# Optimization experiments

Measured on AMD Instinct MI355X. Metric: run time of the kernel, lower is better.

## Reference

```python
import jax, jax.numpy as jnp
import numpy as np

B, D_IN, D_HID, D_OUT = 32768, 512, 1024, 2048

def setup_inputs() -> dict:
    key = jax.random.key(0)
    k1, k2, k3, k4 = jax.random.split(key, 4)
    x = jax.random.normal(k1, (B, D_IN), dtype=jnp.float32)
    # linear1 params (torch Linear default-style init, scale approximated)
    l1_w = jax.random.normal(k2, (D_HID, D_IN), dtype=jnp.float32) * (D_IN ** -0.5)
    l1_b = jax.random.normal(k3, (D_HID,), dtype=jnp.float32) * 0.01
    # second linear params: normal(0, hidden^-0.5) weight, zero bias as in source
    weight = jax.random.normal(k4, (D_OUT, D_HID), dtype=jnp.float32) * (D_HID ** -0.5)
    bias = jnp.zeros((D_OUT,), dtype=jnp.float32)
    return {"x": x, "l1_w": l1_w, "l1_b": l1_b, "weight": weight, "bias": bias}

def reference(x, l1_w, l1_b, weight, bias):
    # linear1: [B, D_IN] -> [B, D_HID]
    h = jnp.einsum('bi,hi->bh', x, l1_w) + l1_b
    # fused linear + max epilogue: scores [B, D_OUT] -> max over output dim
    scores = jnp.einsum('bh,oh->bo', h, weight) + bias
    return jnp.max(scores, axis=-1)  # [B]
```

## Files before the change

### kernel.cpp

```cpp
#include <hip/hip_runtime.h>
#include <hip/hip_bf16.h>
#include <stdint.h>

static constexpr int BATCH = 32768;
static constexpr int DIN   = 512;
static constexpr int DHID  = 1024;
static constexpr int DOUT  = 2048;

typedef __bf16 bf16x8 __attribute__((ext_vector_type(8)));
typedef float  f32x4  __attribute__((ext_vector_type(4)));

__device__ __forceinline__ unsigned short f2bf(float f) {
    unsigned int u = __float_as_uint(f);
    u += 0x7FFFu + ((u >> 16) & 1u);
    return (unsigned short)(u >> 16);
}

__device__ __forceinline__ void gload_lds16(const void* g, void* l) {
    __builtin_amdgcn_global_load_lds((__attribute__((address_space(1))) void*)g,
                                     (__attribute__((address_space(3))) void*)l,
                                     16, 0, 0);
}


__global__ __launch_bounds__(256) void prep_kernel(
    const float* __restrict__ w1, const float4* __restrict__ w2,
    unsigned short* __restrict__ w1t, ushort4* __restrict__ w2b) {
    if (blockIdx.x < 512) {
        __shared__ float tile[32][33];
        const int t     = threadIdx.x;
        const int tileI = blockIdx.x & 15;
        const int tileH = blockIdx.x >> 4;
        const int iBase = tileI * 32, hBase = tileH * 32;
        const int col = t & 31, rowq = t >> 5;
#pragma unroll
        for (int p = 0; p < 4; ++p) {
            const int row = p * 8 + rowq;
            tile[row][col] = w1[(size_t)(hBase + row) * DIN + iBase + col];
        }
        __syncthreads();
#pragma unroll
        for (int p = 0; p < 4; ++p) {
            const int row = p * 8 + rowq;
            w1t[(size_t)(iBase + row) * DHID + hBase + col] = f2bf(tile[col][row]);
        }
    } else {
        const size_t g = (size_t)(blockIdx.x - 512) * 256 + threadIdx.x;
        float4 v = w2[g];
        ushort4 o;
        o.x = f2bf(v.x); o.y = f2bf(v.y); o.z = f2bf(v.z); o.w = f2bf(v.w);
        w2b[g] = o;
    }
}

__global__ __launch_bounds__(256) void bgemv_kernel(
    const float* __restrict__ w2, const float* __restrict__ b1,
    const float* __restrict__ b2, float* __restrict__ bp) {
    const int o    = blockIdx.x * 4 + (threadIdx.x >> 6);
    const int lane = threadIdx.x & 63;
    const float* row = w2 + (size_t)o * DHID;
    float s = 0.f;
#pragma unroll
    for (int j = 0; j < 16; ++j) {
        const int h = j * 64 + lane;
        s += row[h] * b1[h];
    }
#pragma unroll
    for (int off = 1; off < 64; off <<= 1) s += __shfl_xor(s, off);
    if (lane == 0) bp[o] = s + b2[o];
}

__global__ __launch_bounds__(256) void gemmW_kernel(
    const unsigned short* __restrict__ A,
    const unsigned short* __restrict__ Bw,
    unsigned short* __restrict__ W) {
    constexpr int K = DHID;
    __shared__ __align__(16) unsigned short sA[128 * 64];
    __shared__ __align__(16) unsigned short sB[128 * 64];

    const int tid  = threadIdx.x;
    const int lane = tid & 63;
    const int wid  = tid >> 6;
    const int wr = wid >> 1, wc = wid & 1;
    const int r = lane & 15, q = lane >> 4;
    const int sw = r & 7;
    const int blockN = blockIdx.x * 128;
    const int blockM = blockIdx.y * 128;

    const int chKey = (lane & 7) ^ ((lane >> 3) & 7);
    const size_t aBase = (size_t)(blockM + wid * 32 + (lane >> 3)) * K + chKey * 8;
    const size_t bBase = (size_t)(blockN + wid * 32 + (lane >> 3)) * K + chKey * 8;

    f32x4 acc[4][4];
#pragma unroll
    for (int mt = 0; mt < 4; ++mt)
#pragma unroll
        for (int nt = 0; nt < 4; ++nt) { f32x4 z = {0.f, 0.f, 0.f, 0.f}; acc[mt][nt] = z; }

    for (int k0 = 0; k0 < K; k0 += 64) {
#pragma unroll
        for (int j = 0; j < 4; ++j) {
            gload_lds16(A  + aBase + (size_t)j * 8 * K + k0, sA + wid * 2048 + j * 512);
            gload_lds16(Bw + bBase + (size_t)j * 8 * K + k0, sB + wid * 2048 + j * 512);
        }
        __syncthreads();
#pragma unroll
        for (int ks = 0; ks < 2; ++ks) {
            const int ch = ((ks << 2) + q) ^ sw;
            bf16x8 af[4], bf[4];
#pragma unroll
            for (int mt = 0; mt < 4; ++mt) af[mt] = *(const bf16x8*)&sA[(wr * 64 + mt * 16 + r) * 64 + ch * 8];
#pragma unroll
            for (int nt = 0; nt < 4; ++nt) bf[nt] = *(const bf16x8*)&sB[(wc * 64 + nt * 16 + r) * 64 + ch * 8];
#pragma unroll
            for (int mt = 0; mt < 4; ++mt)
#pragma unroll
                for (int nt = 0; nt < 4; ++nt)
                    acc[mt][nt] = __builtin_amdgcn_mfma_f32_16x16x32_bf16(af[mt], bf[nt], acc[mt][nt], 0, 0, 0);
        }
        __syncthreads();
    }

    const int colBase = blockN + wc * 64;
    const int rowBase = blockM + wr * 64;
#pragma unroll
    for (int mt = 0; mt < 4; ++mt) {
        const int row0 = rowBase + mt * 16 + q * 4;
#pragma unroll
        for (int nt = 0; nt < 4; ++nt) {
            const int col = colBase + nt * 16 + r;
#pragma unroll
            for (int reg = 0; reg < 4; ++reg)
                W[(size_t)(row0 + reg) * DIN + col] = f2bf(acc[mt][nt][reg]);
        }
    }
}

__global__ __launch_bounds__(256) void gemmS_kernel(
    const float* __restrict__ X,
    const unsigned short* __restrict__ Bw,
    const float* __restrict__ bp,
    float* __restrict__ partials,
    int mBase) {
    constexpr int K = DIN;
    __shared__ __align__(16) unsigned short sA[128 * 64];
    __shared__ __align__(16) unsigned short sB[128 * 64];

    const int tid  = threadIdx.x;
    const int lane = tid & 63;
    const int wid  = tid >> 6;
    const int wr = wid >> 1, wc = wid & 1;
    const int r = lane & 15, q = lane >> 4;
    const int sw = r & 7;

    const int g    = blockIdx.x;
    const int xcd  = g & 7;
    const int i    = g >> 3;
    const int nIdx = i & 15;
    const int blockM = mBase + (xcd * 16 + (i >> 4)) * 128;
    const int blockN = nIdx * 128;

    int aRow[4], aCh[4], aSlot[4];
#pragma unroll
    for (int j = 0; j < 4; ++j) {
        const int u = j * 256 + tid;
        aRow[j]  = u >> 3;
        aCh[j]   = u & 7;
        aSlot[j] = aRow[j] * 8 + (aCh[j] ^ (aRow[j] & 7));
    }
    const int chKey = (lane & 7) ^ ((lane >> 3) & 7);
    const size_t bBase = (size_t)(blockN + wid * 32 + (lane >> 3)) * K + chKey * 8;

    f32x4 acc[4][4];
#pragma unroll
    for (int mt = 0; mt < 4; ++mt)
#pragma unroll
        for (int nt = 0; nt < 4; ++nt) { f32x4 z = {0.f, 0.f, 0.f, 0.f}; acc[mt][nt] = z; }

    for (int k0 = 0; k0 < K; k0 += 64) {
#pragma unroll
        for (int j = 0; j < 4; ++j)
            gload_lds16(Bw + bBase + (size_t)j * 8 * K + k0, sB + wid * 2048 + j * 512);
#pragma unroll
        for (int j = 0; j < 4; ++j) {
            const float* src = X + (size_t)(blockM + aRow[j]) * K + k0 + aCh[j] * 8;
            f32x4 f0 = *(const f32x4*)src;
            f32x4 f1 = *(const f32x4*)(src + 4);
            bf16x8 v;
#pragma unroll
            for (int i2 = 0; i2 < 4; ++i2) { v[i2] = (__bf16)f0[i2]; v[4 + i2] = (__bf16)f1[i2]; }
            *(bf16x8*)&sA[aSlot[j] * 8] = v;
        }
        __syncthreads();
#pragma unroll
        for (int ks = 0; ks < 2; ++ks) {
            const int ch = ((ks << 2) + q) ^ sw;
            bf16x8 af[4], bf[4];
#pragma unroll
            for (int mt = 0; mt < 4; ++mt) af[mt] = *(const bf16x8*)&sA[(wr * 64 + mt * 16 + r) * 64 + ch * 8];
#pragma unroll
            for (int nt = 0; nt < 4; ++nt) bf[nt] = *(const bf16x8*)&sB[(wc * 64 + nt * 16 + r) * 64 + ch * 8];
#pragma unroll
            for (int mt = 0; mt < 4; ++mt)
#pragma unroll
                for (int nt = 0; nt < 4; ++nt)
                    acc[mt][nt] = __builtin_amdgcn_mfma_f32_16x16x32_bf16(af[mt], bf[nt], acc[mt][nt], 0, 0, 0);
        }
        __syncthreads();
    }

    const int colBase = blockN + wc * 64;
    const int rowBase = blockM + wr * 64;
    float bv[4];
#pragma unroll
    for (int nt = 0; nt < 4; ++nt) bv[nt] = bp[colBase + nt * 16 + r];

    float mx[4][4];
#pragma unroll
    for (int mt = 0; mt < 4; ++mt)
#pragma unroll
        for (int reg = 0; reg < 4; ++reg) {
            float v = acc[mt][0][reg] + bv[0];
            v = fmaxf(v, acc[mt][1][reg] + bv[1]);
            v = fmaxf(v, acc[mt][2][reg] + bv[2]);
            v = fmaxf(v, acc[mt][3][reg] + bv[3]);
            mx[mt][reg] = v;
        }
#pragma unroll
    for (int off = 1; off < 16; off <<= 1)
#pragma unroll
        for (int mt = 0; mt < 4; ++mt)
#pragma unroll
            for (int reg = 0; reg < 4; ++reg)
                mx[mt][reg] = fmaxf(mx[mt][reg], __shfl_xor(mx[mt][reg], off));

    if (r == 0) {
#pragma unroll
        for (int mt = 0; mt < 4; ++mt)
#pragma unroll
            for (int reg = 0; reg < 4; ++reg) {
                const int row = rowBase + mt * 16 + q * 4 + reg;
                partials[(size_t)row * 32 + nIdx * 2 + wc] = mx[mt][reg];
            }
    }
}

__global__ __launch_bounds__(256) void reduce_kernel(
    const float4* __restrict__ partials, float* __restrict__ out) {
    const int row = blockIdx.x * blockDim.x + threadIdx.x;
    const float4* p = partials + (size_t)row * 8;
    float m = -INFINITY;
#pragma unroll
    for (int i = 0; i < 8; ++i) {
        float4 v = p[i];
        m = fmaxf(m, fmaxf(fmaxf(v.x, v.y), fmaxf(v.z, v.w)));
    }
    out[row] = m;
}

extern "C" void kernel_launch(void* const* d_in, const int* in_sizes, int n_in,
                              void* d_out, int out_size, void* d_ws, size_t ws_size,
                              hipStream_t stream) {
    const float* x   = (const float*)d_in[0];
    const float* l1w = (const float*)d_in[1];
    const float* l1b = (const float*)d_in[2];
    const float* w2  = (const float*)d_in[3];
    const float* b2  = (const float*)d_in[4];
    float* out = (float*)d_out;

    char* ws = (char*)d_ws;
    unsigned short* w1t = (unsigned short*)(ws);
    unsigned short* w2b = (unsigned short*)(ws + 1048576);
    unsigned short* Wb  = (unsigned short*)(ws + 5242880);
    float* bp           = (float*)(ws + 7340032);
    float* partials     = (float*)(ws + 7348224);

    prep_kernel<<<2560, 256, 0, stream>>>(l1w, (const float4*)w2, w1t, (ushort4*)w2b);

    bgemv_kernel<<<512, 256, 0, stream>>>(w2, l1b, b2, bp);

    gemmW_kernel<<<dim3(DIN / 128, DOUT / 128), 256, 0, stream>>>(w2b, w1t, Wb);

    gemmS_kernel<<<2048, 256, 0, stream>>>(x, Wb, bp, partials, 0);
    gemmS_kernel<<<2048, 256, 0, stream>>>(x, Wb, bp, partials, BATCH / 2);

    reduce_kernel<<<BATCH / 256, 256, 0, stream>>>((const float4*)partials, out);
}
```

Baseline: 218.8 us.

## Pre-convert x to bf16 in prep kernel, merge bias GEMV, shrink gemmW tiles

The prep kernel now also converts x to bf16 into a workspace buffer and absorbs the bias GEMV, so one launch replaces two. gemmS then loads its A tiles with direct global-to-LDS async loads instead of fp32 register loads plus in-kernel conversion, and runs as a single 4096-block launch instead of two halves. gemmW uses 64x64 tiles so it launches more blocks. The trade-off is an extra full pass over x, reading 64MB of fp32 and writing 32MB of bf16, to make the main GEMM's A-operand loads cheaper.

Result: faster. 203.6 us (-6.9%).

```diff
diff --git a/kernel.cpp b/kernel.cpp
--- a/kernel.cpp
+++ b/kernel.cpp
@@ -24,13 +24,17 @@
 
 
 __global__ __launch_bounds__(256) void prep_kernel(
-    const float* __restrict__ w1, const float4* __restrict__ w2,
-    unsigned short* __restrict__ w1t, ushort4* __restrict__ w2b) {
-    if (blockIdx.x < 512) {
+    const float* __restrict__ w1, const float4* __restrict__ w2f,
+    const float4* __restrict__ xf, const float* __restrict__ b1,
+    const float* __restrict__ b2,
+    unsigned short* __restrict__ w1t, ushort4* __restrict__ w2b,
+    ushort4* __restrict__ xb, float* __restrict__ bp) {
+    const int blk = blockIdx.x;
+    const int t   = threadIdx.x;
+    if (blk < 512) {
         __shared__ float tile[32][33];
-        const int t     = threadIdx.x;
-        const int tileI = blockIdx.x & 15;
-        const int tileH = blockIdx.x >> 4;
+        const int tileI = blk & 15;
+        const int tileH = blk >> 4;
         const int iBase = tileI * 32, hBase = tileH * 32;
         const int col = t & 31, rowq = t >> 5;
 #pragma unroll
@@ -44,30 +48,32 @@
             const int row = p * 8 + rowq;
             w1t[(size_t)(iBase + row) * DHID + hBase + col] = f2bf(tile[col][row]);
         }
-    } else {
-        const size_t g = (size_t)(blockIdx.x - 512) * 256 + threadIdx.x;
-        float4 v = w2[g];
+    } else if (blk < 2560) {
+        const size_t g = (size_t)(blk - 512) * 256 + t;
+        float4 v = w2f[g];
         ushort4 o;
         o.x = f2bf(v.x); o.y = f2bf(v.y); o.z = f2bf(v.z); o.w = f2bf(v.w);
         w2b[g] = o;
-    }
-}
-
-__global__ __launch_bounds__(256) void bgemv_kernel(
-    const float* __restrict__ w2, const float* __restrict__ b1,
-    const float* __restrict__ b2, float* __restrict__ bp) {
-    const int o    = blockIdx.x * 4 + (threadIdx.x >> 6);
-    const int lane = threadIdx.x & 63;
-    const float* row = w2 + (size_t)o * DHID;
-    float s = 0.f;
-#pragma unroll
-    for (int j = 0; j < 16; ++j) {
-        const int h = j * 64 + lane;
-        s += row[h] * b1[h];
-    }
-#pragma unroll
-    for (int off = 1; off < 64; off <<= 1) s += __shfl_xor(s, off);
-    if (lane == 0) bp[o] = s + b2[o];
+    } else if (blk < 18944) {
+        const size_t g = (size_t)(blk - 2560) * 256 + t;
+        float4 v = xf[g];
+        ushort4 o;
+        o.x = f2bf(v.x); o.y = f2bf(v.y); o.z = f2bf(v.z); o.w = f2bf(v.w);
+        xb[g] = o;
+    } else {
+        const int o    = (blk - 18944) * 4 + (t >> 6);
+        const int lane = t & 63;
+        const float* row = (const float*)w2f + (size_t)o * DHID;
+        float s = 0.f;
+#pragma unroll
+        for (int j = 0; j < 16; ++j) {
+            const int h = j * 64 + lane;
+            s += row[h] * b1[h];
+        }
+#pragma unroll
+        for (int off = 1; off < 64; off <<= 1) s += __shfl_xor(s, off);
+        if (lane == 0) bp[o] = s + b2[o];
+    }
 }
 
 __global__ __launch_bounds__(256) void gemmW_kernel(
@@ -75,8 +81,8 @@
     const unsigned short* __restrict__ Bw,
     unsigned short* __restrict__ W) {
     constexpr int K = DHID;
-    __shared__ __align__(16) unsigned short sA[128 * 64];
-    __shared__ __align__(16) unsigned short sB[128 * 64];
+    __shared__ __align__(16) unsigned short sA[64 * 64];
+    __shared__ __align__(16) unsigned short sB[64 * 64];
 
     const int tid  = threadIdx.x;
     const int lane = tid & 63;
@@ -84,51 +90,49 @@
     const int wr = wid >> 1, wc = wid & 1;
     const int r = lane & 15, q = lane >> 4;
     const int sw = r & 7;
-    const int blockN = blockIdx.x * 128;
-    const int blockM = blockIdx.y * 128;
-
-    const int chKey = (lane & 7) ^ ((lane >> 3) & 7);
-    const size_t aBase = (size_t)(blockM + wid * 32 + (lane >> 3)) * K + chKey * 8;
-    const size_t bBase = (size_t)(blockN + wid * 32 + (lane >> 3)) * K + chKey * 8;
-
-    f32x4 acc[4][4];
-#pragma unroll
-    for (int mt = 0; mt < 4; ++mt)
-#pragma unroll
-        for (int nt = 0; nt < 4; ++nt) { f32x4 z = {0.f, 0.f, 0.f, 0.f}; acc[mt][nt] = z; }
+    const int blockN = blockIdx.x * 64;
+    const int blockM = blockIdx.y * 64;
+
+    const int chKey = (lane & 7) ^ (lane >> 3);
+    const size_t aBase = (size_t)(blockM + wid * 8 + (lane >> 3)) * K + chKey * 8;
+    const size_t bBase = (size_t)(blockN + wid * 8 + (lane >> 3)) * K + chKey * 8;
+
+    f32x4 acc[2][2];
+#pragma unroll
+    for (int mt = 0; mt < 2; ++mt)
+#pragma unroll
+        for (int nt = 0; nt < 2; ++nt) { f32x4 z = {0.f, 0.f, 0.f, 0.f}; acc[mt][nt] = z; }
 
     for (int k0 = 0; k0 < K; k0 += 64) {
 #pragma unroll
-        for (int j = 0; j < 4; ++j) {
-            gload_lds16(A  + aBase + (size_t)j * 8 * K + k0, sA + wid * 2048 + j * 512);
-            gload_lds16(Bw + bBase + (size_t)j * 8 * K + k0, sB + wid * 2048 + j * 512);
+        for (int j = 0; j < 2; ++j) {
+            gload_lds16(A  + aBase + (size_t)j * 32 * K + k0, sA + j * 2048 + wid * 512);
+            gload_lds16(Bw + bBase + (size_t)j * 32 * K + k0, sB + j * 2048 + wid * 512);
         }
         __syncthreads();
 #pragma unroll
         for (int ks = 0; ks < 2; ++ks) {
             const int ch = ((ks << 2) + q) ^ sw;
-            bf16x8 af[4], bf[4];
-#pragma unroll
-            for (int mt = 0; mt < 4; ++mt) af[mt] = *(const bf16x8*)&sA[(wr * 64 + mt * 16 + r) * 64 + ch * 8];
-#pragma unroll
-            for (int nt = 0; nt < 4; ++nt) bf[nt] = *(const bf16x8*)&sB[(wc * 64 + nt * 16 + r) * 64 + ch * 8];
-#pragma unroll
-            for (int mt = 0; mt < 4; ++mt)
-#pragma unroll
-                for (int nt = 0; nt < 4; ++nt)
+            bf16x8 af[2], bf[2];
+#pragma unroll
+            for (int mt = 0; mt < 2; ++mt) af[mt] = *(const bf16x8*)&sA[(wr * 32 + mt * 16 + r) * 64 + ch * 8];
+#pragma unroll
+            for (int nt = 0; nt < 2; ++nt) bf[nt] = *(const bf16x8*)&sB[(wc * 32 + nt * 16 + r) * 64 + ch * 8];
+#pragma unroll
+            for (int mt = 0; mt < 2; ++mt)
+#pragma unroll
+                for (int nt = 0; nt < 2; ++nt)
                     acc[mt][nt] = __builtin_amdgcn_mfma_f32_16x16x32_bf16(af[mt], bf[nt], acc[mt][nt], 0, 0, 0);
         }
         __syncthreads();
     }
 
-    const int colBase = blockN + wc * 64;
-    const int rowBase = blockM + wr * 64;
-#pragma unroll
-    for (int mt = 0; mt < 4; ++mt) {
-        const int row0 = rowBase + mt * 16 + q * 4;
-#pragma unroll
-        for (int nt = 0; nt < 4; ++nt) {
-            const int col = colBase + nt * 16 + r;
+#pragma unroll
+    for (int mt = 0; mt < 2; ++mt) {
+        const int row0 = blockM + wr * 32 + mt * 16 + q * 4;
+#pragma unroll
+        for (int nt = 0; nt < 2; ++nt) {
+            const int col = blockN + wc * 32 + nt * 16 + r;
 #pragma unroll
             for (int reg = 0; reg < 4; ++reg)
                 W[(size_t)(row0 + reg) * DIN + col] = f2bf(acc[mt][nt][reg]);
@@ -137,11 +141,10 @@
 }
 
 __global__ __launch_bounds__(256) void gemmS_kernel(
-    const float* __restrict__ X,
+    const unsigned short* __restrict__ A,
     const unsigned short* __restrict__ Bw,
     const float* __restrict__ bp,
-    float* __restrict__ partials,
-    int mBase) {
+    float* __restrict__ partials) {
     constexpr int K = DIN;
     __shared__ __align__(16) unsigned short sA[128 * 64];
     __shared__ __align__(16) unsigned short sB[128 * 64];
@@ -157,18 +160,11 @@
     const int xcd  = g & 7;
     const int i    = g >> 3;
     const int nIdx = i & 15;
-    const int blockM = mBase + (xcd * 16 + (i >> 4)) * 128;
+    const int blockM = (xcd * 32 + (i >> 4)) * 128;
     const int blockN = nIdx * 128;
 
-    int aRow[4], aCh[4], aSlot[4];
-#pragma unroll
-    for (int j = 0; j < 4; ++j) {
-        const int u = j * 256 + tid;
-        aRow[j]  = u >> 3;
-        aCh[j]   = u & 7;
-        aSlot[j] = aRow[j] * 8 + (aCh[j] ^ (aRow[j] & 7));
-    }
-    const int chKey = (lane & 7) ^ ((lane >> 3) & 7);
+    const int chKey = (lane & 7) ^ (lane >> 3);
+    const size_t aBase = (size_t)(blockM + wid * 32 + (lane >> 3)) * K + chKey * 8;
     const size_t bBase = (size_t)(blockN + wid * 32 + (lane >> 3)) * K + chKey * 8;
 
     f32x4 acc[4][4];
@@ -179,17 +175,9 @@
 
     for (int k0 = 0; k0 < K; k0 += 64) {
 #pragma unroll
-        for (int j = 0; j < 4; ++j)
+        for (int j = 0; j < 4; ++j) {
+            gload_lds16(A  + aBase + (size_t)j * 8 * K + k0, sA + wid * 2048 + j * 512);
             gload_lds16(Bw + bBase + (size_t)j * 8 * K + k0, sB + wid * 2048 + j * 512);
-#pragma unroll
-        for (int j = 0; j < 4; ++j) {
-            const float* src = X + (size_t)(blockM + aRow[j]) * K + k0 + aCh[j] * 8;
-            f32x4 f0 = *(const f32x4*)src;
-            f32x4 f1 = *(const f32x4*)(src + 4);
-            bf16x8 v;
-#pragma unroll
-            for (int i2 = 0; i2 < 4; ++i2) { v[i2] = (__bf16)f0[i2]; v[4 + i2] = (__bf16)f1[i2]; }
-            *(bf16x8*)&sA[aSlot[j] * 8] = v;
         }
         __syncthreads();
 #pragma unroll
@@ -273,16 +261,16 @@
     unsigned short* w2b = (unsigned short*)(ws + 1048576);
     unsigned short* Wb  = (unsigned short*)(ws + 5242880);
     float* bp           = (float*)(ws + 7340032);
-    float* partials     = (float*)(ws + 7348224);
-
-    prep_kernel<<<2560, 256, 0, stream>>>(l1w, (const float4*)w2, w1t, (ushort4*)w2b);
-
-    bgemv_kernel<<<512, 256, 0, stream>>>(w2, l1b, b2, bp);
-
-    gemmW_kernel<<<dim3(DIN / 128, DOUT / 128), 256, 0, stream>>>(w2b, w1t, Wb);
-
-    gemmS_kernel<<<2048, 256, 0, stream>>>(x, Wb, bp, partials, 0);
-    gemmS_kernel<<<2048, 256, 0, stream>>>(x, Wb, bp, partials, BATCH / 2);
+    unsigned short* xb  = (unsigned short*)(ws + 7348224);
+    float* partials     = (float*)(ws + 40902656);
+
+    prep_kernel<<<19456, 256, 0, stream>>>(
+        l1w, (const float4*)w2, (const float4*)x, l1b, b2,
+        w1t, (ushort4*)w2b, (ushort4*)xb, bp);
+
+    gemmW_kernel<<<dim3(DIN / 64, DOUT / 64), 256, 0, stream>>>(w2b, w1t, Wb);
+
+    gemmS_kernel<<<4096, 256, 0, stream>>>(xb, Wb, bp, partials);
 
     reduce_kernel<<<BATCH / 256, 256, 0, stream>>>((const float4*)partials, out);
 }
```
